# Optimization experiments

Hardware: AMD Instinct MI355X
Metric: run time of the kernel (lower is better)

Reference implementation:

```python
import jax, jax.numpy as jnp
import numpy as np

B, LQ, LK, D = 16, 32, 256, 512
H, DK = 8, 64
LN_EPS = 1e-5


def _layernorm(x, g, b):
    m = jnp.mean(x, axis=-1, keepdims=True)
    var = jnp.mean(jnp.square(x - m), axis=-1, keepdims=True)
    return (x - m) * jax.lax.rsqrt(var + LN_EPS) * g + b


def setup_inputs() -> dict:
    key = jax.random.key(0)
    ks = jax.random.split(key, 10)
    s = 0.02
    return {
        "q": jax.random.normal(ks[0], (B, LQ, D), jnp.float32),
        "k": jax.random.normal(ks[1], (B, LK, D), jnp.float32),
        "v": jax.random.normal(ks[2], (B, LK, D), jnp.float32),
        "Wq": jax.random.normal(ks[3], (D, D), jnp.float32) * s,
        "Wk": jax.random.normal(ks[4], (D, D), jnp.float32) * s,
        "Wv": jax.random.normal(ks[5], (D, D), jnp.float32) * s,
        "Wfc": jax.random.normal(ks[6], (D, D), jnp.float32) * s,
        "Wg": jax.random.normal(ks[7], (2 * D, D), jnp.float32) * s,
        "bg": jnp.zeros((2 * D,), jnp.float32),
        "Wvp": jax.random.normal(ks[8], (D, D), jnp.float32) * s,
        "bvp": jnp.zeros((D,), jnp.float32),
        "ln1_g": jnp.ones((D,), jnp.float32),
        "ln1_b": jnp.zeros((D,), jnp.float32),
        "ln2_g": jnp.ones((D,), jnp.float32),
        "ln2_b": jnp.zeros((D,), jnp.float32),
    }


def reference(q, k, v, Wq, Wk, Wv, Wfc, Wg, bg, Wvp, bvp, ln1_g, ln1_b, ln2_g, ln2_b):
    # FiLM parameters from queries: [B, LQ, 2D] -> tanh gammas/betas [B, LQ, D]
    film = q @ Wg.T + bg
    gammas, betas = jnp.split(film, 2, axis=-1)
    gammas = jnp.tanh(gammas)
    betas = jnp.tanh(betas)
    # Visual conditioning base: LN(vis_proj(k)) -> [B, LK, D]
    cond_base = _layernorm(k @ Wvp.T + bvp, ln1_g, ln1_b)
    # Per-query modulated keys: broadcast instead of repeat -> [B, LQ, LK, D]
    cond = gammas[:, :, None, :] * cond_base[:, None, :, :] + betas[:, :, None, :]
    cond_k = k[:, None, :, :] + _layernorm(cond, ln2_g, ln2_b)
    # Projections (torch Linear: y = x @ W^T), no qkv bias
    qh = (q @ Wq.T).reshape(B, LQ, H, DK)                 # [B, LQ, H, DK]
    kh = (cond_k @ Wk.T).reshape(B, LQ, LK, H, DK)        # [B, LQ, LK, H, DK]
    vh = (cond_k @ Wv.T).reshape(B, LQ, LK, H, DK)
    # Per-query attention over LK (note: forward arg `v` is unused, as in original)
    scale = DK ** (-0.5)
    logits = jnp.einsum("blhd,blkhd->bhlk", qh, kh) * scale
    weights = jax.nn.softmax(logits, axis=-1)
    # attn_drop/proj_drop are identity in eval mode
    attn = jnp.einsum("bhlk,blkhd->blhd", weights, vh).reshape(B, LQ, H * DK)
    return attn @ Wfc.T
```

## Files before the change

kernel.cpp:

```cpp
#include <hip/hip_runtime.h>
#include <math.h>

namespace {
constexpr float LN_EPS = 1e-5f;

typedef unsigned short u16;
typedef __attribute__((ext_vector_type(8))) short bh8;
typedef __attribute__((ext_vector_type(4))) float fv4;

__device__ __forceinline__ float4 ld4(const float* p) { return *reinterpret_cast<const float4*>(p); }

__device__ __forceinline__ float b2f(u16 x) {
  union { float f; unsigned u; } c; c.u = ((unsigned)x) << 16; return c.f;
}
__device__ __forceinline__ u16 f2b(float f) {
  union { float f; unsigned u; } c; c.f = f;
  unsigned u = c.u;
  u += 0x7FFFu + ((u >> 16) & 1u);
  return (u16)(u >> 16);
}
__device__ __forceinline__ unsigned pk2(float a, float b) {
  return (unsigned)f2b(a) | ((unsigned)f2b(b) << 16);
}
__device__ __forceinline__ uint4 pack8(const float* v) {
  uint4 r; r.x = pk2(v[0], v[1]); r.y = pk2(v[2], v[3]); r.z = pk2(v[4], v[5]); r.w = pk2(v[6], v[7]);
  return r;
}

__device__ __forceinline__ bh8 lds_rd(const u16* S, int row, int c8) {
  return *(const bh8*)&S[row * 64 + ((c8 ^ (row & 7)) << 3)];
}

struct FA {
  const float *q, *k, *Wq, *Wk, *Wv, *Wfc, *Wg, *bg, *Wvp, *bvp;
  const float *ln1g, *ln1b, *ln2g, *ln2b;
  float* out;
  u16 *WkT_bf, *Wv_bf, *Wfc_bf, *k_bf, *kT_bf, *qh_bf;
  float *gam, *bet, *condpre;
  u16 *cb_bf, *cbT_bf, *u_bf, *w1_bf;
  float *c2, *c3, *c4;
  u16* A96_bf;
  float *sum_be, *sum_be2, *P;
  u16* s_bf;
  u16 *cbsq_bf, *w_bf, *W1_bf;
  float *S1, *S2;
  u16* attn_bf;
  float *K1, *K2;
};

struct GA {
  const u16* A; const u16* B; const u16* Balt;
  long lda, ldb, sAz, sBz;
  float* Cf; u16* Cb; u16* Cb2;
  long ldc, sCz;
  int M, K, epi;
  const float* e0; const float* e1;
};

__device__ __forceinline__ void gemm_core(const GA& a, u16* As, u16* Bs,
                                          int bx, int by, int bz, int t) {
  const int z = bz;
  const int bm0 = bx * 64, bn0 = by * 64;
  const int lane = t & 63, w = t >> 6;
  const int wm = (w >> 1) * 32, wn = (w & 1) * 32;
  const u16* Ab = a.A + (long)z * a.sAz;
  const u16* Bbase = (a.Balt != nullptr && bm0 >= 64) ? a.Balt : a.B;
  const u16* Bb = Bbase + (long)z * a.sBz;

  const int sr = t >> 3, sc8 = t & 7, sc = sc8 * 8;
  int ar0 = bm0 + sr;      if (ar0 > a.M - 1) ar0 = a.M - 1;
  int ar1 = bm0 + sr + 32; if (ar1 > a.M - 1) ar1 = a.M - 1;
  const u16* ap0 = Ab + (long)ar0 * a.lda + sc;
  const u16* ap1 = Ab + (long)ar1 * a.lda + sc;
  const u16* bp0 = Bb + (long)(bn0 + sr) * a.ldb + sc;
  const u16* bp1 = Bb + (long)(bn0 + sr + 32) * a.ldb + sc;
  const int iA0 = sr * 64 + ((sc8 ^ (sr & 7)) << 3);
  const int iA1 = iA0 + 32 * 64;

  fv4 zero = {0.f, 0.f, 0.f, 0.f};
  fv4 acc00 = zero, acc01 = zero, acc10 = zero, acc11 = zero;
  const int r0 = lane & 15, kq8 = lane >> 4;
  const int nk = a.K >> 6;

  uint4 av0 = *(const uint4*)ap0, av1 = *(const uint4*)ap1;
  uint4 bv0 = *(const uint4*)bp0, bv1 = *(const uint4*)bp1;
  for (int kt = 0; kt < nk; ++kt) {
    __syncthreads();
    *(uint4*)&As[iA0] = av0; *(uint4*)&As[iA1] = av1;
    *(uint4*)&Bs[iA0] = bv0; *(uint4*)&Bs[iA1] = bv1;
    __syncthreads();
    if (kt + 1 < nk) {
      ap0 += 64; ap1 += 64; bp0 += 64; bp1 += 64;
      av0 = *(const uint4*)ap0; av1 = *(const uint4*)ap1;
      bv0 = *(const uint4*)bp0; bv1 = *(const uint4*)bp1;
    }
#pragma unroll
    for (int kc = 0; kc < 2; ++kc) {
      const int c8 = kq8 + 4 * kc;
      bh8 aa0 = lds_rd(As, wm + r0, c8);
      bh8 aa1 = lds_rd(As, wm + 16 + r0, c8);
      bh8 bb0 = lds_rd(Bs, wn + r0, c8);
      bh8 bb1 = lds_rd(Bs, wn + 16 + r0, c8);
      acc00 = __builtin_amdgcn_mfma_f32_16x16x32_bf16(aa0, bb0, acc00, 0, 0, 0);
      acc01 = __builtin_amdgcn_mfma_f32_16x16x32_bf16(aa0, bb1, acc01, 0, 0, 0);
      acc10 = __builtin_amdgcn_mfma_f32_16x16x32_bf16(aa1, bb0, acc10, 0, 0, 0);
      acc11 = __builtin_amdgcn_mfma_f32_16x16x32_bf16(aa1, bb1, acc11, 0, 0, 0);
    }
  }

  fv4 accs[2][2] = {{acc00, acc01}, {acc10, acc11}};
#pragma unroll
  for (int rb = 0; rb < 2; ++rb) {
#pragma unroll
    for (int cbl = 0; cbl < 2; ++cbl) {
#pragma unroll
      for (int j = 0; j < 4; ++j) {
        const int r = bm0 + wm + rb * 16 + (lane >> 4) * 4 + j;
        const int c = bn0 + wn + cbl * 16 + (lane & 15);
        if (r >= a.M) continue;
        const float v = accs[rb][cbl][j];
        if (a.epi == 0) {
          a.Cf[(long)z * a.sCz + (long)r * a.ldc + c] = v;
        } else if (a.epi == 1) {
          a.Cb[(long)z * a.sCz + (long)r * a.ldc + c] = f2b(v);
        } else if (a.epi == 5) {
          a.Cb[((long)r * 8 + z) * a.ldc + c] = f2b(v * 0.125f);
        } else {
          const u16 ub = f2b(v * 0.125f);
          const long orow = (long)r * 8 + z;
          a.Cb[orow * 512 + c] = ub;
          const float uu = b2f(ub);
          const float t1 = a.e1[c] * uu;
          a.Cb2[orow * 512 + c] = f2b(a.e0[(long)r * 512 + c] * t1);
        }
      }
    }
  }
}

struct GAF {
  const float* Af; const float* Bf;
  long lda, ldb;
  float* Cf; u16* Cb; float* Cf2;
  long ldc;
  int M, K, epi;
  const float* e0;
};

__device__ __forceinline__ void gemm_core_f32(const GAF& a, u16* As, u16* Bs,
                                              int bx, int by, int t) {
  const int bm0 = bx * 64, bn0 = by * 64;
  const int lane = t & 63, w = t >> 6;
  const int wm = (w >> 1) * 32, wn = (w & 1) * 32;
  const int sr = t >> 3, sc8 = t & 7, sc = sc8 * 8;
  int ar0 = bm0 + sr;      if (ar0 > a.M - 1) ar0 = a.M - 1;
  int ar1 = bm0 + sr + 32; if (ar1 > a.M - 1) ar1 = a.M - 1;
  const float* ap0 = a.Af + (long)ar0 * a.lda + sc;
  const float* ap1 = a.Af + (long)ar1 * a.lda + sc;
  const float* bp0 = a.Bf + (long)(bn0 + sr) * a.ldb + sc;
  const float* bp1 = a.Bf + (long)(bn0 + sr + 32) * a.ldb + sc;
  const int iA0 = sr * 64 + ((sc8 ^ (sr & 7)) << 3);
  const int iA1 = iA0 + 32 * 64;

  fv4 zero = {0.f, 0.f, 0.f, 0.f};
  fv4 acc00 = zero, acc01 = zero, acc10 = zero, acc11 = zero;
  const int r0 = lane & 15, kq8 = lane >> 4;
  const int nk = a.K >> 6;

  float4 xa0 = ld4(ap0), xa1 = ld4(ap0 + 4), xa2 = ld4(ap1), xa3 = ld4(ap1 + 4);
  float4 xb0 = ld4(bp0), xb1 = ld4(bp0 + 4), xb2 = ld4(bp1), xb3 = ld4(bp1 + 4);
  for (int kt = 0; kt < nk; ++kt) {
    __syncthreads();
    {
      const float v0[8] = {xa0.x, xa0.y, xa0.z, xa0.w, xa1.x, xa1.y, xa1.z, xa1.w};
      const float v1[8] = {xa2.x, xa2.y, xa2.z, xa2.w, xa3.x, xa3.y, xa3.z, xa3.w};
      const float v2[8] = {xb0.x, xb0.y, xb0.z, xb0.w, xb1.x, xb1.y, xb1.z, xb1.w};
      const float v3[8] = {xb2.x, xb2.y, xb2.z, xb2.w, xb3.x, xb3.y, xb3.z, xb3.w};
      *(uint4*)&As[iA0] = pack8(v0);
      *(uint4*)&As[iA1] = pack8(v1);
      *(uint4*)&Bs[iA0] = pack8(v2);
      *(uint4*)&Bs[iA1] = pack8(v3);
    }
    __syncthreads();
    if (kt + 1 < nk) {
      ap0 += 64; ap1 += 64; bp0 += 64; bp1 += 64;
      xa0 = ld4(ap0); xa1 = ld4(ap0 + 4); xa2 = ld4(ap1); xa3 = ld4(ap1 + 4);
      xb0 = ld4(bp0); xb1 = ld4(bp0 + 4); xb2 = ld4(bp1); xb3 = ld4(bp1 + 4);
    }
#pragma unroll
    for (int kc = 0; kc < 2; ++kc) {
      const int c8 = kq8 + 4 * kc;
      bh8 aa0 = lds_rd(As, wm + r0, c8);
      bh8 aa1 = lds_rd(As, wm + 16 + r0, c8);
      bh8 bb0 = lds_rd(Bs, wn + r0, c8);
      bh8 bb1 = lds_rd(Bs, wn + 16 + r0, c8);
      acc00 = __builtin_amdgcn_mfma_f32_16x16x32_bf16(aa0, bb0, acc00, 0, 0, 0);
      acc01 = __builtin_amdgcn_mfma_f32_16x16x32_bf16(aa0, bb1, acc01, 0, 0, 0);
      acc10 = __builtin_amdgcn_mfma_f32_16x16x32_bf16(aa1, bb0, acc10, 0, 0, 0);
      acc11 = __builtin_amdgcn_mfma_f32_16x16x32_bf16(aa1, bb1, acc11, 0, 0, 0);
    }
  }

  fv4 accs[2][2] = {{acc00, acc01}, {acc10, acc11}};
#pragma unroll
  for (int rb = 0; rb < 2; ++rb) {
#pragma unroll
    for (int cbl = 0; cbl < 2; ++cbl) {
#pragma unroll
      for (int j = 0; j < 4; ++j) {
        const int r = bm0 + wm + rb * 16 + (lane >> 4) * 4 + j;
        const int c = bn0 + wn + cbl * 16 + (lane & 15);
        if (r >= a.M) continue;
        const float v = accs[rb][cbl][j];
        if (a.epi == 1) {
          a.Cb[(long)r * a.ldc + c] = f2b(v);
        } else if (a.epi == 2) {
          const float x = tanhf(v + a.e0[c]);
          if (c < 512) a.Cf[(long)r * 512 + c] = x;
          else         a.Cf2[(long)r * 512 + (c - 512)] = x;
        } else {
          a.Cf[(long)r * a.ldc + c] = v + a.e0[c];
        }
      }
    }
  }
}

struct GA2 {
  const u16* A1; const u16* A2; const u16* B1; const u16* B2;
  long lda, ldb, sAz, sBz;
  float* Cf; float* Cf2; u16* Cb;
  long ldc, sCz;
  int M, K;
  const float* e1; const float* e2; const float* e3;
  const float* e4; const float* e5; const float* e6;
};

__device__ __forceinline__ void gemm2_core(const GA2& a, u16* As1, u16* As2,
                                           u16* Bs1, u16* Bs2,
                                           int bx, int by, int bz, int t, int EPI) {
  const int z = bz;
  const int bm0 = bx * 64, bn0 = by * 64;
  const int lane = t & 63, w = t >> 6;
  const int wm = (w >> 1) * 32, wn = (w & 1) * 32;
  const u16* A1b = a.A1 + (long)z * a.sAz;
  const u16* A2b = a.A2 + (long)z * a.sAz;
  const u16* B1b = a.B1 + (long)z * a.sBz;
  const u16* B2b = a.B2 + (long)z * a.sBz;

  const int sr = t >> 3, sc8 = t & 7, sc = sc8 * 8;
  const long aoff0 = (long)(bm0 + sr) * a.lda + sc;
  const long aoff1 = (long)(bm0 + sr + 32) * a.lda + sc;
  const long boff0 = (long)(bn0 + sr) * a.ldb + sc;
  const long boff1 = (long)(bn0 + sr + 32) * a.ldb + sc;
  const u16 *a1p0 = A1b + aoff0, *a1p1 = A1b + aoff1;
  const u16 *a2p0 = A2b + aoff0, *a2p1 = A2b + aoff1;
  const u16 *b1p0 = B1b + boff0, *b1p1 = B1b + boff1;
  const u16 *b2p0 = B2b + boff0, *b2p1 = B2b + boff1;
  const int iA0 = sr * 64 + ((sc8 ^ (sr & 7)) << 3);
  const int iA1 = iA0 + 32 * 64;

  fv4 zero = {0.f, 0.f, 0.f, 0.f};
  fv4 p00 = zero, p01 = zero, p10 = zero, p11 = zero;
  fv4 q00 = zero, q01 = zero, q10 = zero, q11 = zero;
  const int r0 = lane & 15, kq8 = lane >> 4;
  const int nk = a.K >> 6;

  uint4 a1v0 = *(const uint4*)a1p0, a1v1 = *(const uint4*)a1p1;
  uint4 a2v0 = *(const uint4*)a2p0, a2v1 = *(const uint4*)a2p1;
  uint4 b1v0 = *(const uint4*)b1p0, b1v1 = *(const uint4*)b1p1;
  uint4 b2v0 = *(const uint4*)b2p0, b2v1 = *(const uint4*)b2p1;
  for (int kt = 0; kt < nk; ++kt) {
    __syncthreads();
    *(uint4*)&As1[iA0] = a1v0; *(uint4*)&As1[iA1] = a1v1;
    *(uint4*)&As2[iA0] = a2v0; *(uint4*)&As2[iA1] = a2v1;
    *(uint4*)&Bs1[iA0] = b1v0; *(uint4*)&Bs1[iA1] = b1v1;
    *(uint4*)&Bs2[iA0] = b2v0; *(uint4*)&Bs2[iA1] = b2v1;
    __syncthreads();
    if (kt + 1 < nk) {
      a1p0 += 64; a1p1 += 64; a2p0 += 64; a2p1 += 64;
      b1p0 += 64; b1p1 += 64; b2p0 += 64; b2p1 += 64;
      a1v0 = *(const uint4*)a1p0; a1v1 = *(const uint4*)a1p1;
      a2v0 = *(const uint4*)a2p0; a2v1 = *(const uint4*)a2p1;
      b1v0 = *(const uint4*)b1p0; b1v1 = *(const uint4*)b1p1;
      b2v0 = *(const uint4*)b2p0; b2v1 = *(const uint4*)b2p1;
    }
#pragma unroll
    for (int kc = 0; kc < 2; ++kc) {
      const int c8 = kq8 + 4 * kc;
      bh8 x0 = lds_rd(As1, wm + r0, c8);
      bh8 x1 = lds_rd(As1, wm + 16 + r0, c8);
      bh8 y0 = lds_rd(Bs1, wn + r0, c8);
      bh8 y1 = lds_rd(Bs1, wn + 16 + r0, c8);
      p00 = __builtin_amdgcn_mfma_f32_16x16x32_bf16(x0, y0, p00, 0, 0, 0);
      p01 = __builtin_amdgcn_mfma_f32_16x16x32_bf16(x0, y1, p01, 0, 0, 0);
      p10 = __builtin_amdgcn_mfma_f32_16x16x32_bf16(x1, y0, p10, 0, 0, 0);
      p11 = __builtin_amdgcn_mfma_f32_16x16x32_bf16(x1, y1, p11, 0, 0, 0);
      bh8 u0 = lds_rd(As2, wm + r0, c8);
      bh8 u1 = lds_rd(As2, wm + 16 + r0, c8);
      bh8 v0 = lds_rd(Bs2, wn + r0, c8);
      bh8 v1 = lds_rd(Bs2, wn + 16 + r0, c8);
      q00 = __builtin_amdgcn_mfma_f32_16x16x32_bf16(u0, v0, q00, 0, 0, 0);
      q01 = __builtin_amdgcn_mfma_f32_16x16x32_bf16(u0, v1, q01, 0, 0, 0);
      q10 = __builtin_amdgcn_mfma_f32_16x16x32_bf16(u1, v0, q10, 0, 0, 0);
      q11 = __builtin_amdgcn_mfma_f32_16x16x32_bf16(u1, v1, q11, 0, 0, 0);
    }
  }

  fv4 pa[2][2] = {{p00, p01}, {p10, p11}};
  fv4 qa[2][2] = {{q00, q01}, {q10, q11}};
#pragma unroll
  for (int rb = 0; rb < 2; ++rb) {
#pragma unroll
    for (int cbl = 0; cbl < 2; ++cbl) {
#pragma unroll
      for (int j = 0; j < 4; ++j) {
        const int r = bm0 + wm + rb * 16 + (lane >> 4) * 4 + j;
        const int c = bn0 + wn + cbl * 16 + (lane & 15);
        if (r >= a.M) continue;
        const float v1 = pa[rb][cbl][j];
        const float v2 = qa[rb][cbl][j];
        if (EPI == 2) {
          const long idx = (long)z * a.sCz + (long)r * a.ldc + c;
          a.Cf[idx] = v1;
          a.Cf2[idx] = v2;
        } else {
          const int lh = z * 256 + r;
          const int bl = z * 32 + (r >> 3);
          const float G2d = a.e1[c], B2d = a.e2[c];
          const float gv = a.e3[(long)bl * 512 + c];
          const float bev = a.e4[(long)bl * 512 + c];
          const float sv = v1 + B2d + G2d * (gv * v2 + bev * a.e5[lh] - a.e6[lh]);
          a.Cb[(long)z * a.sCz + (long)r * a.ldc + c] = f2b(sv);
        }
      }
    }
  }
}

__device__ __forceinline__ void tpf32_unit(const float* src, long lds, u16* dst, long ldd,
                                           int tr, int tc, int t, float T[64][65]) {
  const int c = t & 63, rg = t >> 6;
#pragma unroll 4
  for (int i = 0; i < 16; ++i) {
    const int r = rg + 4 * i;
    T[r][c] = src[(long)(tr * 64 + r) * lds + tc * 64 + c];
  }
  __syncthreads();
#pragma unroll 4
  for (int i = 0; i < 16; ++i) {
    const int r = rg + 4 * i;
    dst[(long)(tc * 64 + r) * ldd + tr * 64 + c] = f2b(T[c][r]);
  }
}

__device__ __forceinline__ void tpb16_unit(const u16* src, u16* dst, int b, int w32,
                                           int t, float T[64][65]) {
  const int tr = w32 >> 3, tc = w32 & 7;
  const u16* s = src + (long)b * 131072;
  u16* d = dst + (long)b * 131072;
  const int c = t & 63, rg = t >> 6;
#pragma unroll 4
  for (int i = 0; i < 16; ++i) {
    const int r = rg + 4 * i;
    T[r][c] = b2f(s[(long)(tr * 64 + r) * 512 + tc * 64 + c]);
  }
  __syncthreads();
#pragma unroll 4
  for (int i = 0; i < 16; ++i) {
    const int r = rg + 4 * i;
    d[(long)(tc * 64 + r) * 256 + tr * 64 + c] = f2b(T[c][r]);
  }
}

__device__ __forceinline__ void cvt_unit(const float* s, u16* d, long blk, int t) {
  const long idx = blk * 2048 + t * 8;
  const float4 x0 = ld4(s + idx), x1 = ld4(s + idx + 4);
  const float v[8] = {x0.x, x0.y, x0.z, x0.w, x1.x, x1.y, x1.z, x1.w};
  *(uint4*)(d + idx) = pack8(v);
}

__device__ __forceinline__ void ln_unit(const FA& f, int u, int t) {
  const int lane = t & 63, e = lane * 8;
  const int row = u * 4 + (t >> 6);
  const float* p = f.condpre + (long)row * 512 + e;
  const float4 x0 = ld4(p), x1 = ld4(p + 4);
  float v[8] = {x0.x, x0.y, x0.z, x0.w, x1.x, x1.y, x1.z, x1.w};
  float s = 0.f, sq = 0.f;
#pragma unroll
  for (int i = 0; i < 8; ++i) { s += v[i]; sq += v[i] * v[i]; }
#pragma unroll
  for (int m = 1; m < 64; m <<= 1) { s += __shfl_xor(s, m); sq += __shfl_xor(sq, m); }
  const float mu = s * (1.f / 512.f);
  const float iv = rsqrtf(sq * (1.f / 512.f) - mu * mu + LN_EPS);
  const float4 g0 = ld4(f.ln1g + e), g1 = ld4(f.ln1g + e + 4);
  const float4 b0 = ld4(f.ln1b + e), b1 = ld4(f.ln1b + e + 4);
  const float gg[8] = {g0.x, g0.y, g0.z, g0.w, g1.x, g1.y, g1.z, g1.w};
  const float bb[8] = {b0.x, b0.y, b0.z, b0.w, b1.x, b1.y, b1.z, b1.w};
  float o[8], osq[8];
#pragma unroll
  for (int i = 0; i < 8; ++i) {
    o[i] = (v[i] - mu) * iv * gg[i] + bb[i];
    osq[i] = o[i] * o[i];
  }
  *(uint4*)(f.cb_bf + (long)row * 512 + e) = pack8(o);
  *(uint4*)(f.cbsq_bf + (long)row * 512 + e) = pack8(osq);
}

__device__ __forceinline__ void a96_unit(const FA& f, int u, int t) {
  const int lane = t & 63, e = lane * 8;
  const int bl = u * 4 + (t >> 6);
  const int b = bl >> 5, l = bl & 31;
  const float4 ga0 = ld4(f.gam + (long)bl * 512 + e), ga1 = ld4(f.gam + (long)bl * 512 + e + 4);
  const float4 be0 = ld4(f.bet + (long)bl * 512 + e), be1 = ld4(f.bet + (long)bl * 512 + e + 4);
  const float gv[8] = {ga0.x, ga0.y, ga0.z, ga0.w, ga1.x, ga1.y, ga1.z, ga1.w};
  const float bv[8] = {be0.x, be0.y, be0.z, be0.w, be1.x, be1.y, be1.z, be1.w};
  float gg[8], gb[8]; float s1 = 0.f, s2 = 0.f;
#pragma unroll
  for (int i = 0; i < 8; ++i) {
    gg[i] = gv[i] * gv[i]; gb[i] = gv[i] * bv[i];
    s1 += bv[i]; s2 += bv[i] * bv[i];
  }
  const long basei = ((long)b * 96 + l) * 512 + e;
  *(uint4*)(f.A96_bf + basei) = pack8(gv);
  *(uint4*)(f.A96_bf + basei + 32 * 512) = pack8(gb);
  *(uint4*)(f.A96_bf + basei + 64 * 512) = pack8(gg);
#pragma unroll
  for (int m = 1; m < 64; m <<= 1) { s1 += __shfl_xor(s1, m); s2 += __shfl_xor(s2, m); }
  if (lane == 0) { f.sum_be[bl] = s1; f.sum_be2[bl] = s2; }
}

__device__ __forceinline__ void csum_unit(const FA& f, int u, int t) {
  const int lane = t & 63, e = lane * 8;
  const int lh = u * 4 + (t >> 6);
  const int bl = lh >> 3;
  const uint4 up = *(const uint4*)(f.u_bf + (long)lh * 512 + e);
  const u16* us = (const u16*)&up;
  const float4 be0 = ld4(f.bet + (long)bl * 512 + e), be1 = ld4(f.bet + (long)bl * 512 + e + 4);
  const float4 G0 = ld4(f.ln2g + e), G1 = ld4(f.ln2g + e + 4);
  const float4 B0 = ld4(f.ln2b + e), B1 = ld4(f.ln2b + e + 4);
  const float bv[8] = {be0.x, be0.y, be0.z, be0.w, be1.x, be1.y, be1.z, be1.w};
  const float Gv[8] = {G0.x, G0.y, G0.z, G0.w, G1.x, G1.y, G1.z, G1.w};
  const float Bv[8] = {B0.x, B0.y, B0.z, B0.w, B1.x, B1.y, B1.z, B1.w};
  float a2 = 0.f, a3 = 0.f, a4 = 0.f;
#pragma unroll
  for (int i = 0; i < 8; ++i) {
    const float uu = b2f(us[i]);
    const float t1 = Gv[i] * uu;
    a2 += bv[i] * t1; a3 += t1; a4 += Bv[i] * uu;
  }
#pragma unroll
  for (int m = 1; m < 64; m <<= 1) {
    a2 += __shfl_xor(a2, m); a3 += __shfl_xor(a3, m); a4 += __shfl_xor(a4, m);
  }
  if (lane == 0) { f.c2[lh] = a2; f.c3[lh] = a3; f.c4[lh] = a4; }
}

__device__ __forceinline__ void softmax2_unit(const FA& f, int u, int t) {
  const int lane = t & 63, e = lane * 4;
  const int lh = u * 4 + (t >> 6);
  const int b = lh >> 8, l = (lh >> 3) & 31, bl = lh >> 3;
  const float4 k1 = ld4(f.K1 + (long)lh * 256 + e);
  const float4 k2 = ld4(f.K2 + (long)lh * 256 + e);
  const float* Pb = f.P + ((long)b * 96 + l) * 256 + e;
  const float4 p0 = ld4(Pb), pgb = ld4(Pb + 32 * 256), pg2 = ld4(Pb + 64 * 256);
  const float sbe = f.sum_be[bl], sbe2 = f.sum_be2[bl];
  const float C2 = f.c2[lh], C3 = f.c3[lh], C4 = f.c4[lh];
  const float k1s[4] = {k1.x, k1.y, k1.z, k1.w};
  const float k2s[4] = {k2.x, k2.y, k2.z, k2.w};
  const float p0s[4] = {p0.x, p0.y, p0.z, p0.w};
  const float pgbs[4] = {pgb.x, pgb.y, pgb.z, pgb.w};
  const float pg2s[4] = {pg2.x, pg2.y, pg2.z, pg2.w};
  float mu[4], iv[4], lgs[4];
#pragma unroll
  for (int i = 0; i < 4; ++i) {
    mu[i] = (p0s[i] + sbe) * (1.f / 512.f);
    const float msq = (pg2s[i] + 2.f * pgbs[i] + sbe2) * (1.f / 512.f);
    iv[i] = rsqrtf(msq - mu[i] * mu[i] + LN_EPS);
    lgs[i] = k1s[i] + C4 + iv[i] * (k2s[i] + C2 - mu[i] * C3);
  }
  float mx = fmaxf(fmaxf(lgs[0], lgs[1]), fmaxf(lgs[2], lgs[3]));
#pragma unroll
  for (int m = 1; m < 64; m <<= 1) mx = fmaxf(mx, __shfl_xor(mx, m));
  float ex[4]; float z = 0.f;
#pragma unroll
  for (int i = 0; i < 4; ++i) { ex[i] = expf(lgs[i] - mx); z += ex[i]; }
#pragma unroll
  for (int m = 1; m < 64; m <<= 1) z += __shfl_xor(z, m);
  const float rz = 1.f / z;
  float wv[4], w1v[4]; float s1 = 0.f, s2 = 0.f;
#pragma unroll
  for (int i = 0; i < 4; ++i) {
    wv[i] = ex[i] * rz;
    w1v[i] = wv[i] * iv[i];
    s1 += w1v[i]; s2 += w1v[i] * mu[i];
  }
  uint2 wp, w1p;
  wp.x = pk2(wv[0], wv[1]); wp.y = pk2(wv[2], wv[3]);
  w1p.x = pk2(w1v[0], w1v[1]); w1p.y = pk2(w1v[2], w1v[3]);
  *(uint2*)(f.w_bf + (long)lh * 256 + e) = wp;
  *(uint2*)(f.W1_bf + (long)lh * 256 + e) = w1p;
#pragma unroll
  for (int m = 1; m < 64; m <<= 1) { s1 += __shfl_xor(s1, m); s2 += __shfl_xor(s2, m); }
  if (lane == 0) { f.S1[lh] = s1; f.S2[lh] = s2; }
}

__global__ __launch_bounds__(256) void pA_k(FA f) {
  __shared__ __align__(16) char smem[16704];
  u16* As = (u16*)smem;
  u16* Bs = (u16*)(smem + 8192);
  float (*T)[65] = (float(*)[65])smem;
  const int u = blockIdx.x, t = threadIdx.x;
  if (u < 512) {
    GAF a = {}; a.Af = f.k; a.Bf = f.Wvp; a.lda = 512; a.ldb = 512;
    a.Cf = f.condpre; a.ldc = 512; a.M = 4096; a.K = 512; a.epi = 4; a.e0 = f.bvp;
    gemm_core_f32(a, As, Bs, u % 64, u / 64, t);
  } else if (u < 640) {
    const int r = u - 512;
    GAF a = {}; a.Af = f.q; a.Bf = f.Wg; a.lda = 512; a.ldb = 512;
    a.Cf = f.gam; a.Cf2 = f.bet; a.ldc = 512; a.M = 512; a.K = 512; a.epi = 2; a.e0 = f.bg;
    gemm_core_f32(a, As, Bs, r % 8, r / 8, t);
  } else if (u < 704) {
    const int r = u - 640;
    GAF a = {}; a.Af = f.q; a.Bf = f.Wq; a.lda = 512; a.ldb = 512;
    a.Cb = f.qh_bf; a.ldc = 512; a.M = 512; a.K = 512; a.epi = 1;
    gemm_core_f32(a, As, Bs, r % 8, r / 8, t);
  } else if (u < 1728) {
    cvt_unit(f.k, f.k_bf, u - 704, t);
  } else if (u < 1856) {
    cvt_unit(f.Wv, f.Wv_bf, u - 1728, t);
  } else if (u < 1984) {
    cvt_unit(f.Wfc, f.Wfc_bf, u - 1856, t);
  } else if (u < 2048) {
    const int tt = u - 1984;
    tpf32_unit(f.Wk, 512, f.WkT_bf, 512, tt >> 3, tt & 7, t, T);
  } else {
    const int tt = u - 2048;
    const int b = tt >> 5, w32 = tt & 31;
    tpf32_unit(f.k + (long)b * 131072, 512, f.kT_bf + (long)b * 131072, 256,
               w32 >> 3, w32 & 7, t, T);
  }
}

__global__ __launch_bounds__(256) void pB_k(FA f) {
  __shared__ __align__(16) char smem[16384];
  u16* As = (u16*)smem;
  u16* Bs = (u16*)(smem + 8192);
  const int u = blockIdx.x, t = threadIdx.x;
  if (u < 1024) {
    ln_unit(f, u, t);
  } else if (u < 1152) {
    a96_unit(f, u - 1024, t);
  } else {
    const int r = u - 1152;
    GA a = {}; a.A = f.qh_bf; a.lda = 512; a.sAz = 64;
    a.B = f.WkT_bf; a.ldb = 512; a.sBz = 64;
    a.Cb = f.u_bf; a.Cb2 = f.w1_bf; a.ldc = 512; a.M = 512; a.K = 64; a.epi = 6;
    a.e0 = f.gam; a.e1 = f.ln2g;
    gemm_core(a, As, Bs, r % 8, (r / 8) % 8, r / 64, t);
  }
}

__global__ __launch_bounds__(256) void pC_k(FA f) {
  __shared__ __align__(16) char smem[32768];
  const int u = blockIdx.x, t = threadIdx.x;
  if (u < 128) {
    u16* As = (u16*)smem; u16* Bs = (u16*)(smem + 8192);
    GA a = {}; a.A = f.A96_bf; a.lda = 512; a.sAz = 96 * 512;
    a.B = f.cb_bf; a.Balt = f.cbsq_bf; a.ldb = 512; a.sBz = 256 * 512;
    a.Cf = f.P; a.ldc = 256; a.sCz = 96 * 256; a.M = 96; a.K = 512; a.epi = 0;
    gemm_core(a, As, Bs, u % 2, (u / 2) % 4, u / 8, t);
  } else if (u < 640) {
    float (*T)[65] = (float(*)[65])smem;
    const int tt = u - 128;
    tpb16_unit(f.cb_bf, f.cbT_bf, tt >> 5, tt & 31, t, T);
  } else if (u < 1664) {
    csum_unit(f, u - 640, t);
  } else {
    const int r = u - 1664;
    u16* As1 = (u16*)smem; u16* As2 = (u16*)(smem + 8192);
    u16* Bs1 = (u16*)(smem + 16384); u16* Bs2 = (u16*)(smem + 24576);
    GA2 d = {};
    d.A1 = f.u_bf; d.A2 = f.w1_bf; d.B1 = f.k_bf; d.B2 = f.cb_bf;
    d.lda = 512; d.ldb = 512; d.sAz = 256 * 512; d.sBz = 256 * 512;
    d.Cf = f.K1; d.Cf2 = f.K2; d.ldc = 256; d.sCz = 256 * 256; d.M = 256; d.K = 512;
    gemm2_core(d, As1, As2, Bs1, Bs2, r % 4, (r / 4) % 4, r / 16, t, 2);
  }
}

__global__ __launch_bounds__(256) void pD_k(FA f) {
  softmax2_unit(f, blockIdx.x, threadIdx.x);
}

__global__ __launch_bounds__(256) void pE_k(FA f) {
  __shared__ __align__(16) char smem[32768];
  u16* As1 = (u16*)smem; u16* As2 = (u16*)(smem + 8192);
  u16* Bs1 = (u16*)(smem + 16384); u16* Bs2 = (u16*)(smem + 24576);
  const int u = blockIdx.x, t = threadIdx.x;
  GA2 d = {};
  d.A1 = f.w_bf; d.A2 = f.W1_bf; d.B1 = f.kT_bf; d.B2 = f.cbT_bf;
  d.lda = 256; d.ldb = 256; d.sAz = 256 * 256; d.sBz = 512 * 256;
  d.Cb = f.s_bf; d.ldc = 512; d.sCz = 256 * 512; d.M = 256; d.K = 256;
  d.e1 = f.ln2g; d.e2 = f.ln2b; d.e3 = f.gam; d.e4 = f.bet; d.e5 = f.S1; d.e6 = f.S2;
  gemm2_core(d, As1, As2, Bs1, Bs2, u % 4, (u / 4) % 8, u / 32, t, 1);
}

__global__ __launch_bounds__(256) void pF_k(FA f) {
  __shared__ __align__(16) char smem[16384];
  u16* As = (u16*)smem; u16* Bs = (u16*)(smem + 8192);
  const int u = blockIdx.x, t = threadIdx.x;
  GA a = {}; a.A = f.s_bf; a.lda = 4096; a.sAz = 512;
  a.B = f.Wv_bf; a.ldb = 512; a.sBz = 64 * 512;
  a.Cb = f.attn_bf; a.ldc = 512; a.sCz = 64; a.M = 512; a.K = 512; a.epi = 1;
  gemm_core(a, As, Bs, u % 8, 0, u / 8, t);
}

__global__ __launch_bounds__(256) void pG_k(FA f) {
  __shared__ __align__(16) char smem[16384];
  u16* As = (u16*)smem; u16* Bs = (u16*)(smem + 8192);
  const int u = blockIdx.x, t = threadIdx.x;
  GA a = {}; a.A = f.attn_bf; a.lda = 512;
  a.B = f.Wfc_bf; a.ldb = 512;
  a.Cf = f.out; a.ldc = 512; a.M = 512; a.K = 512; a.epi = 0;
  gemm_core(a, As, Bs, u % 8, u / 8, 0, t);
}

}

extern "C" void kernel_launch(void* const* d_in, const int* in_sizes, int n_in,
                              void* d_out, int out_size, void* d_ws, size_t ws_size,
                              hipStream_t stream) {
  (void)in_sizes; (void)n_in; (void)out_size;
  FA fa;
  fa.q    = (const float*)d_in[0];
  fa.k    = (const float*)d_in[1];
  fa.Wq   = (const float*)d_in[3];
  fa.Wk   = (const float*)d_in[4];
  fa.Wv   = (const float*)d_in[5];
  fa.Wfc  = (const float*)d_in[6];
  fa.Wg   = (const float*)d_in[7];
  fa.bg   = (const float*)d_in[8];
  fa.Wvp  = (const float*)d_in[9];
  fa.bvp  = (const float*)d_in[10];
  fa.ln1g = (const float*)d_in[11];
  fa.ln1b = (const float*)d_in[12];
  fa.ln2g = (const float*)d_in[13];
  fa.ln2b = (const float*)d_in[14];
  fa.out  = (float*)d_out;

  char* base = (char*)d_ws;
  size_t off = 0;
  auto au16 = [&](size_t n) -> u16* {
    u16* p = (u16*)(base + off); off = (off + n * 2 + 255) & ~(size_t)255; return p;
  };
  auto af32 = [&](size_t n) -> float* {
    float* p = (float*)(base + off); off = (off + n * 4 + 255) & ~(size_t)255; return p;
  };
  (void)au16(262144);
  (void)au16(524288);
  (void)au16(262144);
  (void)au16(262144);
  fa.WkT_bf  = au16(262144);
  fa.Wv_bf   = au16(262144);
  fa.Wfc_bf  = au16(262144);
  fa.k_bf    = au16(2097152);
  fa.kT_bf   = au16(2097152);
  fa.qh_bf   = au16(262144);
  fa.gam     = af32(262144);
  fa.bet     = af32(262144);
  fa.condpre = af32(2097152);
  fa.cb_bf   = au16(2097152);
  fa.cbT_bf  = au16(2097152);
  fa.u_bf    = au16(2097152);
  fa.w1_bf   = au16(2097152);
  fa.c2      = af32(4096);
  fa.c3      = af32(4096);
  fa.c4      = af32(4096);
  fa.A96_bf  = au16(16 * 96 * 512);
  fa.sum_be  = af32(512);
  fa.sum_be2 = af32(512);
  fa.P       = af32(16 * 96 * 256);
  float* sbuf   = af32(1048576);
  float* logits = af32(1048576);
  fa.w_bf    = au16(1048576);
  fa.W1_bf   = au16(1048576);
  fa.S1      = af32(4096);
  fa.S2      = af32(4096);
  fa.attn_bf = au16(262144);
  const size_t need = off;
  fa.s_bf    = (u16*)sbuf;
  fa.cbsq_bf = (u16*)logits;
  fa.K1      = fa.condpre;
  fa.K2      = fa.condpre + 1048576;

  if (ws_size < need) return;

  const dim3 blk(256);
  pA_k<<<dim3(2560), blk, 0, stream>>>(fa);
  pB_k<<<dim3(1664), blk, 0, stream>>>(fa);
  pC_k<<<dim3(1920), blk, 0, stream>>>(fa);
  pD_k<<<dim3(1024), blk, 0, stream>>>(fa);
  pE_k<<<dim3(512),  blk, 0, stream>>>(fa);
  pF_k<<<dim3(64),   blk, 0, stream>>>(fa);
  pG_k<<<dim3(64),   blk, 0, stream>>>(fa);
}
```

Baseline: 82.29 us.

## Fuse softmax stage into the attention-weight GEMM kernel

Removes the separate softmax kernel (pD) and recomputes logits, softmax and the inverse-std weighting inside each pE block. The normalized weights go into LDS as bf16 rather than round-tripping w_bf/W1_bf/S1/S2 through global memory. The iv-scaled second operand is built on the fly from LDS before the MFMA. This saves a launch and global traffic, but each of the 8 column blocks now recomputes softmax for its rows, using two passes over K1/K2/P, which adds redundant work.

```diff
diff --git a/kernel.cpp b/kernel.cpp
--- a/kernel.cpp
+++ b/kernel.cpp
@@ -42,8 +42,7 @@
   u16* A96_bf;
   float *sum_be, *sum_be2, *P;
   u16* s_bf;
-  u16 *cbsq_bf, *w_bf, *W1_bf;
-  float *S1, *S2;
+  u16 *cbsq_bf;
   u16* attn_bf;
   float *K1, *K2;
 };
@@ -229,16 +228,14 @@
 struct GA2 {
   const u16* A1; const u16* A2; const u16* B1; const u16* B2;
   long lda, ldb, sAz, sBz;
-  float* Cf; float* Cf2; u16* Cb;
+  float* Cf; float* Cf2;
   long ldc, sCz;
   int M, K;
-  const float* e1; const float* e2; const float* e3;
-  const float* e4; const float* e5; const float* e6;
 };
 
 __device__ __forceinline__ void gemm2_core(const GA2& a, u16* As1, u16* As2,
                                            u16* Bs1, u16* Bs2,
-                                           int bx, int by, int bz, int t, int EPI) {
+                                           int bx, int by, int bz, int t) {
   const int z = bz;
   const int bm0 = bx * 64, bn0 = by * 64;
   const int lane = t & 63, w = t >> 6;
@@ -317,22 +314,9 @@
       for (int j = 0; j < 4; ++j) {
         const int r = bm0 + wm + rb * 16 + (lane >> 4) * 4 + j;
         const int c = bn0 + wn + cbl * 16 + (lane & 15);
-        if (r >= a.M) continue;
-        const float v1 = pa[rb][cbl][j];
-        const float v2 = qa[rb][cbl][j];
-        if (EPI == 2) {
-          const long idx = (long)z * a.sCz + (long)r * a.ldc + c;
-          a.Cf[idx] = v1;
-          a.Cf2[idx] = v2;
-        } else {
-          const int lh = z * 256 + r;
-          const int bl = z * 32 + (r >> 3);
-          const float G2d = a.e1[c], B2d = a.e2[c];
-          const float gv = a.e3[(long)bl * 512 + c];
-          const float bev = a.e4[(long)bl * 512 + c];
-          const float sv = v1 + B2d + G2d * (gv * v2 + bev * a.e5[lh] - a.e6[lh]);
-          a.Cb[(long)z * a.sCz + (long)r * a.ldc + c] = f2b(sv);
-        }
+        const long idx = (long)z * a.sCz + (long)r * a.ldc + c;
+        a.Cf[idx] = pa[rb][cbl][j];
+        a.Cf2[idx] = qa[rb][cbl][j];
       }
     }
   }
@@ -454,55 +438,6 @@
     a2 += __shfl_xor(a2, m); a3 += __shfl_xor(a3, m); a4 += __shfl_xor(a4, m);
   }
   if (lane == 0) { f.c2[lh] = a2; f.c3[lh] = a3; f.c4[lh] = a4; }
-}
-
-__device__ __forceinline__ void softmax2_unit(const FA& f, int u, int t) {
-  const int lane = t & 63, e = lane * 4;
-  const int lh = u * 4 + (t >> 6);
-  const int b = lh >> 8, l = (lh >> 3) & 31, bl = lh >> 3;
-  const float4 k1 = ld4(f.K1 + (long)lh * 256 + e);
-  const float4 k2 = ld4(f.K2 + (long)lh * 256 + e);
-  const float* Pb = f.P + ((long)b * 96 + l) * 256 + e;
-  const float4 p0 = ld4(Pb), pgb = ld4(Pb + 32 * 256), pg2 = ld4(Pb + 64 * 256);
-  const float sbe = f.sum_be[bl], sbe2 = f.sum_be2[bl];
-  const float C2 = f.c2[lh], C3 = f.c3[lh], C4 = f.c4[lh];
-  const float k1s[4] = {k1.x, k1.y, k1.z, k1.w};
-  const float k2s[4] = {k2.x, k2.y, k2.z, k2.w};
-  const float p0s[4] = {p0.x, p0.y, p0.z, p0.w};
-  const float pgbs[4] = {pgb.x, pgb.y, pgb.z, pgb.w};
-  const float pg2s[4] = {pg2.x, pg2.y, pg2.z, pg2.w};
-  float mu[4], iv[4], lgs[4];
-#pragma unroll
-  for (int i = 0; i < 4; ++i) {
-    mu[i] = (p0s[i] + sbe) * (1.f / 512.f);
-    const float msq = (pg2s[i] + 2.f * pgbs[i] + sbe2) * (1.f / 512.f);
-    iv[i] = rsqrtf(msq - mu[i] * mu[i] + LN_EPS);
-    lgs[i] = k1s[i] + C4 + iv[i] * (k2s[i] + C2 - mu[i] * C3);
-  }
-  float mx = fmaxf(fmaxf(lgs[0], lgs[1]), fmaxf(lgs[2], lgs[3]));
-#pragma unroll
-  for (int m = 1; m < 64; m <<= 1) mx = fmaxf(mx, __shfl_xor(mx, m));
-  float ex[4]; float z = 0.f;
-#pragma unroll
-  for (int i = 0; i < 4; ++i) { ex[i] = expf(lgs[i] - mx); z += ex[i]; }
-#pragma unroll
-  for (int m = 1; m < 64; m <<= 1) z += __shfl_xor(z, m);
-  const float rz = 1.f / z;
-  float wv[4], w1v[4]; float s1 = 0.f, s2 = 0.f;
-#pragma unroll
-  for (int i = 0; i < 4; ++i) {
-    wv[i] = ex[i] * rz;
-    w1v[i] = wv[i] * iv[i];
-    s1 += w1v[i]; s2 += w1v[i] * mu[i];
-  }
-  uint2 wp, w1p;
-  wp.x = pk2(wv[0], wv[1]); wp.y = pk2(wv[2], wv[3]);
-  w1p.x = pk2(w1v[0], w1v[1]); w1p.y = pk2(w1v[2], w1v[3]);
-  *(uint2*)(f.w_bf + (long)lh * 256 + e) = wp;
-  *(uint2*)(f.W1_bf + (long)lh * 256 + e) = w1p;
-#pragma unroll
-  for (int m = 1; m < 64; m <<= 1) { s1 += __shfl_xor(s1, m); s2 += __shfl_xor(s2, m); }
-  if (lane == 0) { f.S1[lh] = s1; f.S2[lh] = s2; }
 }
 
 __global__ __launch_bounds__(256) void pA_k(FA f) {
@@ -584,25 +519,196 @@
     d.A1 = f.u_bf; d.A2 = f.w1_bf; d.B1 = f.k_bf; d.B2 = f.cb_bf;
     d.lda = 512; d.ldb = 512; d.sAz = 256 * 512; d.sBz = 256 * 512;
     d.Cf = f.K1; d.Cf2 = f.K2; d.ldc = 256; d.sCz = 256 * 256; d.M = 256; d.K = 512;
-    gemm2_core(d, As1, As2, Bs1, Bs2, r % 4, (r / 4) % 4, r / 16, t, 2);
-  }
-}
-
-__global__ __launch_bounds__(256) void pD_k(FA f) {
-  softmax2_unit(f, blockIdx.x, threadIdx.x);
+    gemm2_core(d, As1, As2, Bs1, Bs2, r % 4, (r / 4) % 4, r / 16, t);
+  }
 }
 
 __global__ __launch_bounds__(256) void pE_k(FA f) {
-  __shared__ __align__(16) char smem[32768];
-  u16* As1 = (u16*)smem; u16* As2 = (u16*)(smem + 8192);
-  u16* Bs1 = (u16*)(smem + 16384); u16* Bs2 = (u16*)(smem + 24576);
+  __shared__ __align__(16) u16 w_lds[4 * 64 * 64];
+  __shared__ float iv_lds[8][256];
+  __shared__ float s1_lds[64], s2_lds[64];
+  __shared__ __align__(16) u16 Bs1[64 * 64];
+  __shared__ __align__(16) u16 Bs2[64 * 64];
+
   const int u = blockIdx.x, t = threadIdx.x;
-  GA2 d = {};
-  d.A1 = f.w_bf; d.A2 = f.W1_bf; d.B1 = f.kT_bf; d.B2 = f.cbT_bf;
-  d.lda = 256; d.ldb = 256; d.sAz = 256 * 256; d.sBz = 512 * 256;
-  d.Cb = f.s_bf; d.ldc = 512; d.sCz = 256 * 512; d.M = 256; d.K = 256;
-  d.e1 = f.ln2g; d.e2 = f.ln2b; d.e3 = f.gam; d.e4 = f.bet; d.e5 = f.S1; d.e6 = f.S2;
-  gemm2_core(d, As1, As2, Bs1, Bs2, u % 4, (u / 4) % 8, u / 32, t, 1);
+  const int bx = u & 3, by = (u >> 2) & 7, z = u >> 5;
+  const int bm0 = bx * 64, bn0 = by * 64;
+
+  {
+    const int row = t >> 2, qq = t & 3;
+    const int r = bm0 + row;
+    const int lh = z * 256 + r;
+    const int bl = z * 32 + (r >> 3);
+    const int l = (r >> 3) & 31;
+    const float* k1p = f.K1 + (long)lh * 256 + qq * 64;
+    const float* k2p = f.K2 + (long)lh * 256 + qq * 64;
+    const float* Pb  = f.P + ((long)z * 96 + l) * 256 + qq * 64;
+    const float sbe = f.sum_be[bl], sbe2 = f.sum_be2[bl];
+    const float C2 = f.c2[lh], C3 = f.c3[lh], C4 = f.c4[lh];
+
+    float mx = -3.4e38f;
+    for (int j = 0; j < 64; j += 4) {
+      const float4 k1 = ld4(k1p + j), k2 = ld4(k2p + j);
+      const float4 p0 = ld4(Pb + j), pgb = ld4(Pb + 8192 + j), pg2 = ld4(Pb + 16384 + j);
+      const float k1s[4] = {k1.x, k1.y, k1.z, k1.w};
+      const float k2s[4] = {k2.x, k2.y, k2.z, k2.w};
+      const float p0s[4] = {p0.x, p0.y, p0.z, p0.w};
+      const float pgbs[4] = {pgb.x, pgb.y, pgb.z, pgb.w};
+      const float pg2s[4] = {pg2.x, pg2.y, pg2.z, pg2.w};
+#pragma unroll
+      for (int i = 0; i < 4; ++i) {
+        const float mu = (p0s[i] + sbe) * (1.f / 512.f);
+        const float msq = (pg2s[i] + 2.f * pgbs[i] + sbe2) * (1.f / 512.f);
+        const float iv = rsqrtf(msq - mu * mu + LN_EPS);
+        const float lg = k1s[i] + C4 + iv * (k2s[i] + C2 - mu * C3);
+        mx = fmaxf(mx, lg);
+      }
+    }
+    mx = fmaxf(mx, __shfl_xor(mx, 1));
+    mx = fmaxf(mx, __shfl_xor(mx, 2));
+
+    float zs = 0.f, a1 = 0.f, a2 = 0.f;
+    const int rsw = row & 7;
+    for (int j8 = 0; j8 < 64; j8 += 8) {
+      float exv[8], ivv[8];
+#pragma unroll
+      for (int h4 = 0; h4 < 2; ++h4) {
+        const int j = j8 + h4 * 4;
+        const float4 k1 = ld4(k1p + j), k2 = ld4(k2p + j);
+        const float4 p0 = ld4(Pb + j), pgb = ld4(Pb + 8192 + j), pg2 = ld4(Pb + 16384 + j);
+        const float k1s[4] = {k1.x, k1.y, k1.z, k1.w};
+        const float k2s[4] = {k2.x, k2.y, k2.z, k2.w};
+        const float p0s[4] = {p0.x, p0.y, p0.z, p0.w};
+        const float pgbs[4] = {pgb.x, pgb.y, pgb.z, pgb.w};
+        const float pg2s[4] = {pg2.x, pg2.y, pg2.z, pg2.w};
+#pragma unroll
+        for (int i = 0; i < 4; ++i) {
+          const float mu = (p0s[i] + sbe) * (1.f / 512.f);
+          const float msq = (pg2s[i] + 2.f * pgbs[i] + sbe2) * (1.f / 512.f);
+          const float iv = rsqrtf(msq - mu * mu + LN_EPS);
+          const float lg = k1s[i] + C4 + iv * (k2s[i] + C2 - mu * C3);
+          const float ex = expf(lg - mx);
+          zs += ex;
+          a1 += ex * iv;
+          a2 += ex * iv * mu;
+          exv[h4 * 4 + i] = ex;
+          ivv[h4 * 4 + i] = iv;
+        }
+      }
+      *(uint4*)&w_lds[qq * 4096 + row * 64 + (((j8 >> 3) ^ rsw) << 3)] = pack8(exv);
+      if ((row & 7) == 0) {
+        *(float4*)&iv_lds[row >> 3][qq * 64 + j8] = make_float4(ivv[0], ivv[1], ivv[2], ivv[3]);
+        *(float4*)&iv_lds[row >> 3][qq * 64 + j8 + 4] = make_float4(ivv[4], ivv[5], ivv[6], ivv[7]);
+      }
+    }
+    zs += __shfl_xor(zs, 1); zs += __shfl_xor(zs, 2);
+    a1 += __shfl_xor(a1, 1); a1 += __shfl_xor(a1, 2);
+    a2 += __shfl_xor(a2, 1); a2 += __shfl_xor(a2, 2);
+    const float rz = 1.f / zs;
+    if (qq == 0) { s1_lds[row] = a1 * rz; s2_lds[row] = a2 * rz; }
+
+    for (int j8 = 0; j8 < 64; j8 += 8) {
+      u16* slot = &w_lds[qq * 4096 + row * 64 + (((j8 >> 3) ^ rsw) << 3)];
+      uint4 pk = *(uint4*)slot;
+      const u16* pe = (const u16*)&pk;
+      float sv[8];
+#pragma unroll
+      for (int e = 0; e < 8; ++e) sv[e] = b2f(pe[e]) * rz;
+      *(uint4*)slot = pack8(sv);
+    }
+  }
+
+  const int lane = t & 63, w = t >> 6;
+  const int wm = (w >> 1) * 32, wn = (w & 1) * 32;
+  const u16* B1b = f.kT_bf + (long)z * (512 * 256);
+  const u16* B2b = f.cbT_bf + (long)z * (512 * 256);
+  const int srb = t >> 3, sc8 = t & 7, sc = sc8 * 8;
+  const int iB0 = srb * 64 + ((sc8 ^ (srb & 7)) << 3);
+  const int iB1 = iB0 + 32 * 64;
+  const u16* b1p0 = B1b + (long)(bn0 + srb) * 256 + sc;
+  const u16* b1p1 = B1b + (long)(bn0 + srb + 32) * 256 + sc;
+  const u16* b2p0 = B2b + (long)(bn0 + srb) * 256 + sc;
+  const u16* b2p1 = B2b + (long)(bn0 + srb + 32) * 256 + sc;
+
+  fv4 zero = {0.f, 0.f, 0.f, 0.f};
+  fv4 p00 = zero, p01 = zero, p10 = zero, p11 = zero;
+  fv4 q00 = zero, q01 = zero, q10 = zero, q11 = zero;
+  const int r0 = lane & 15, kq8 = lane >> 4;
+  const int rowA0 = wm + r0, rowA1 = wm + 16 + r0;
+  const float* ivA0 = &iv_lds[rowA0 >> 3][0];
+  const float* ivA1 = &iv_lds[rowA1 >> 3][0];
+
+  uint4 b1v0 = *(const uint4*)b1p0, b1v1 = *(const uint4*)b1p1;
+  uint4 b2v0 = *(const uint4*)b2p0, b2v1 = *(const uint4*)b2p1;
+  for (int kt = 0; kt < 4; ++kt) {
+    __syncthreads();
+    *(uint4*)&Bs1[iB0] = b1v0; *(uint4*)&Bs1[iB1] = b1v1;
+    *(uint4*)&Bs2[iB0] = b2v0; *(uint4*)&Bs2[iB1] = b2v1;
+    __syncthreads();
+    if (kt + 1 < 4) {
+      b1p0 += 64; b1p1 += 64; b2p0 += 64; b2p1 += 64;
+      b1v0 = *(const uint4*)b1p0; b1v1 = *(const uint4*)b1p1;
+      b2v0 = *(const uint4*)b2p0; b2v1 = *(const uint4*)b2p1;
+    }
+    const u16* wp = &w_lds[kt * 4096];
+#pragma unroll
+    for (int kc = 0; kc < 2; ++kc) {
+      const int c8 = kq8 + 4 * kc;
+      const int ko = kt * 64 + c8 * 8;
+      bh8 x0 = lds_rd(wp, rowA0, c8);
+      bh8 x1 = lds_rd(wp, rowA1, c8);
+      bh8 y0 = lds_rd(Bs1, wn + r0, c8);
+      bh8 y1 = lds_rd(Bs1, wn + 16 + r0, c8);
+      p00 = __builtin_amdgcn_mfma_f32_16x16x32_bf16(x0, y0, p00, 0, 0, 0);
+      p01 = __builtin_amdgcn_mfma_f32_16x16x32_bf16(x0, y1, p01, 0, 0, 0);
+      p10 = __builtin_amdgcn_mfma_f32_16x16x32_bf16(x1, y0, p10, 0, 0, 0);
+      p11 = __builtin_amdgcn_mfma_f32_16x16x32_bf16(x1, y1, p11, 0, 0, 0);
+      const float4 i00 = ld4(ivA0 + ko), i01 = ld4(ivA0 + ko + 4);
+      const float4 i10 = ld4(ivA1 + ko), i11 = ld4(ivA1 + ko + 4);
+      const float iv0[8] = {i00.x, i00.y, i00.z, i00.w, i01.x, i01.y, i01.z, i01.w};
+      const float iv1[8] = {i10.x, i10.y, i10.z, i10.w, i11.x, i11.y, i11.z, i11.w};
+      const u16* x0p = (const u16*)&x0;
+      const u16* x1p = (const u16*)&x1;
+      float w0[8], w1v[8];
+#pragma unroll
+      for (int e = 0; e < 8; ++e) {
+        w0[e] = b2f(x0p[e]) * iv0[e];
+        w1v[e] = b2f(x1p[e]) * iv1[e];
+      }
+      uint4 u0u = pack8(w0); bh8 u0 = *(bh8*)&u0u;
+      uint4 u1u = pack8(w1v); bh8 u1 = *(bh8*)&u1u;
+      bh8 v0 = lds_rd(Bs2, wn + r0, c8);
+      bh8 v1 = lds_rd(Bs2, wn + 16 + r0, c8);
+      q00 = __builtin_amdgcn_mfma_f32_16x16x32_bf16(u0, v0, q00, 0, 0, 0);
+      q01 = __builtin_amdgcn_mfma_f32_16x16x32_bf16(u0, v1, q01, 0, 0, 0);
+      q10 = __builtin_amdgcn_mfma_f32_16x16x32_bf16(u1, v0, q10, 0, 0, 0);
+      q11 = __builtin_amdgcn_mfma_f32_16x16x32_bf16(u1, v1, q11, 0, 0, 0);
+    }
+  }
+
+  fv4 pa[2][2] = {{p00, p01}, {p10, p11}};
+  fv4 qa[2][2] = {{q00, q01}, {q10, q11}};
+#pragma unroll
+  for (int rb = 0; rb < 2; ++rb) {
+#pragma unroll
+    for (int cbl = 0; cbl < 2; ++cbl) {
+#pragma unroll
+      for (int j = 0; j < 4; ++j) {
+        const int rl = wm + rb * 16 + (lane >> 4) * 4 + j;
+        const int rg = bm0 + rl;
+        const int c = bn0 + wn + cbl * 16 + (lane & 15);
+        const int lh = z * 256 + rg;
+        const int bl = z * 32 + (rg >> 3);
+        const float G2d = f.ln2g[c], B2d = f.ln2b[c];
+        const float gv = f.gam[(long)bl * 512 + c];
+        const float bev = f.bet[(long)bl * 512 + c];
+        const float sv = pa[rb][cbl][j] + B2d +
+                         G2d * (gv * qa[rb][cbl][j] + bev * s1_lds[rl] - s2_lds[rl]);
+        f.s_bf[(long)z * (256 * 512) + (long)rg * 512 + c] = f2b(sv);
+        (void)lh;
+      }
+    }
+  }
 }
 
 __global__ __launch_bounds__(256) void pF_k(FA f) {
@@ -682,10 +788,10 @@
   fa.P       = af32(16 * 96 * 256);
   float* sbuf   = af32(1048576);
   float* logits = af32(1048576);
-  fa.w_bf    = au16(1048576);
-  fa.W1_bf   = au16(1048576);
-  fa.S1      = af32(4096);
-  fa.S2      = af32(4096);
+  (void)au16(1048576);
+  (void)au16(1048576);
+  (void)af32(4096);
+  (void)af32(4096);
   fa.attn_bf = au16(262144);
   const size_t need = off;
   fa.s_bf    = (u16*)sbuf;
@@ -699,7 +805,6 @@
   pA_k<<<dim3(2560), blk, 0, stream>>>(fa);
   pB_k<<<dim3(1664), blk, 0, stream>>>(fa);
   pC_k<<<dim3(1920), blk, 0, stream>>>(fa);
-  pD_k<<<dim3(1024), blk, 0, stream>>>(fa);
   pE_k<<<dim3(512),  blk, 0, stream>>>(fa);
   pF_k<<<dim3(64),   blk, 0, stream>>>(fa);
   pG_k<<<dim3(64),   blk, 0, stream>>>(fa);
```

New measurement: 112.2 us. 36.3% more time.
